# Optimization experiments

Measured on AMD Instinct MI355X. Metric: run time of the kernel, lower is better.

## Reference

```python
import jax, jax.numpy as jnp
import numpy as np
import math

B, L, D = 2, 2048, 512
D_INNER, D_STATE, D_CONV = 2 * D, 16, 4
DT_RANK = math.ceil(D / 16)  # 32


def setup_inputs() -> dict:
    key = jax.random.key(0)
    ks = jax.random.split(key, 9)
    s = 0.02
    x = jax.random.normal(ks[0], (B, L, D), dtype=jnp.float32)
    W_in = jax.random.normal(ks[1], (D, 2 * D_INNER), dtype=jnp.float32) * s
    conv_w = jax.random.normal(ks[2], (D_INNER, D_CONV), dtype=jnp.float32) * s
    conv_b = jnp.zeros((D_INNER,), dtype=jnp.float32)
    W_x = jax.random.normal(ks[3], (D_INNER, DT_RANK + 2 * D_STATE), dtype=jnp.float32) * s
    W_dt = jax.random.normal(ks[4], (DT_RANK, D_INNER), dtype=jnp.float32) * s
    b_dt = jax.random.normal(ks[5], (D_INNER,), dtype=jnp.float32) * s
    # S4D-real init: A = -[1..d_state] per channel
    A_log = jnp.log(jnp.broadcast_to(jnp.arange(1, D_STATE + 1, dtype=jnp.float32), (D_INNER, D_STATE)))
    D_param = jnp.ones((D_INNER,), dtype=jnp.float32)
    W_out = jax.random.normal(ks[6], (D_INNER, D), dtype=jnp.float32) * s
    return {"x": x, "W_in": W_in, "conv_w": conv_w, "conv_b": conv_b,
            "W_x": W_x, "W_dt": W_dt, "b_dt": b_dt, "A_log": A_log,
            "D_param": D_param, "W_out": W_out}


def _mamba(x, W_in, conv_w, conv_b, W_x, W_dt, b_dt, A_log, D_param, W_out):
    # in_proj -> [u, z]
    xz = jnp.einsum('bld,de->ble', x, W_in)
    u, z = jnp.split(xz, 2, axis=-1)  # each (B, L, d_inner)
    # depthwise causal conv1d along L
    u_c = jnp.transpose(u, (0, 2, 1))  # (B, d_inner, L)
    kern = conv_w[:, None, :]          # (d_inner, 1, d_conv)
    u_c = jax.lax.conv_general_dilated(
        u_c, kern, window_strides=(1,), padding=[(D_CONV - 1, 0)],
        feature_group_count=D_INNER,
        dimension_numbers=('NCH', 'OIH', 'NCH')) + conv_b[None, :, None]
    u = jax.nn.silu(jnp.transpose(u_c, (0, 2, 1)))  # (B, L, d_inner)
    # input-dependent dt, B, C
    x_dbl = jnp.einsum('bld,de->ble', u, W_x)
    dt_r = x_dbl[..., :DT_RANK]
    Bm = x_dbl[..., DT_RANK:DT_RANK + D_STATE]          # (B, L, d_state)
    Cm = x_dbl[..., DT_RANK + D_STATE:]                  # (B, L, d_state)
    dt = jax.nn.softplus(jnp.einsum('blr,rd->bld', dt_r, W_dt) + b_dt)  # (B, L, d_inner)
    A = -jnp.exp(A_log)  # (d_inner, d_state)

    def step(h, inp):
        dt_t, B_t, C_t, u_t = inp  # (B,d_inner), (B,d_state), (B,d_state), (B,d_inner)
        dA = jnp.exp(dt_t[:, :, None] * A)                      # (B, d_inner, d_state)
        h = h * dA + (dt_t * u_t)[:, :, None] * B_t[:, None, :]
        y = jnp.einsum('bds,bs->bd', h, C_t)
        return h, y

    h0 = jnp.zeros((B, D_INNER, D_STATE), dtype=x.dtype)
    xs = (jnp.transpose(dt, (1, 0, 2)), jnp.transpose(Bm, (1, 0, 2)),
          jnp.transpose(Cm, (1, 0, 2)), jnp.transpose(u, (1, 0, 2)))
    _, ys = jax.lax.scan(step, h0, xs)
    y = jnp.transpose(ys, (1, 0, 2)) + u * D_param  # (B, L, d_inner)
    y = y * jax.nn.silu(z)
    return jnp.einsum('bld,de->ble', y, W_out)


def reference(x, W_in, conv_w, conv_b, W_x, W_dt, b_dt, A_log, D_param, W_out):
    # MambaLayer.forward (eval): out = x + drop_path(mamba(x)); drop_path == Identity at eval
    return x + _mamba(x, W_in, conv_w, conv_b, W_x, W_dt, b_dt, A_log, D_param, W_out)
```

## Files before the change

### kernel.cpp

```cpp
#include <hip/hip_runtime.h>
#include <math.h>

#define BB 2
#define LL 2048
#define DD 512
#define DIN 1024
#define DXZ 2048
#define DSTATE 16
#define DTRANK 32
#define NDBL 64
#define ML (BB*LL)
#define LC3 32
#define NCH3 64
#define CP3 36
#define PHS 17

typedef __bf16 bf16_t;
typedef bf16_t bf16x8 __attribute__((ext_vector_type(8)));
typedef bf16_t bf16x4 __attribute__((ext_vector_type(4)));
typedef float f32x4 __attribute__((ext_vector_type(4)));

#define GBK 64

typedef const __attribute__((address_space(1))) void* gp1_t;
typedef __attribute__((address_space(3))) void* lp3_t;

__device__ __forceinline__ float fast_silu(float x) {
  return x * __builtin_amdgcn_rcpf(1.f + __builtin_amdgcn_exp2f(-1.44269504f * x));
}

template <int TM, int TN, int MODE, int CT>
__launch_bounds__(256)
__global__ void gemm_mfma(const bf16_t* __restrict__ A,
                          const bf16_t* __restrict__ Bt,
                          float* __restrict__ C, int ldc,
                          int M, int N, int K, int gx,
                          const float* __restrict__ aux) {
  constexpr int ABYTES = 2 * TM * GBK * 2;
  constexpr int BBYTES = 2 * TN * GBK * 2;
  __shared__ __align__(16) char smem[ABYTES + BBYTES];
  bf16_t* As = (bf16_t*)smem;
  bf16_t* Bs = (bf16_t*)(smem + ABYTES);
  const int tid = threadIdx.x;
  const int wid = tid >> 6, lane = tid & 63;
  const int q = lane >> 4, ln = lane & 15;
  constexpr int WM = TM / 2, WN = TN / 2;
  constexpr int FM = WM / 16, FN = WN / 16;
  constexpr int AI = TM * GBK / 2048;
  constexpr int BI = TN * GBK / 2048;
  constexpr int SN = AI + BI;
  const int wm = (wid >> 1) * WM, wn = (wid & 1) * WN;

  const int nwg = gridDim.x;
  const int cpx = nwg >> 3;
  const int o = blockIdx.x;
  const int wg = (o & 7) * cpx + (o >> 3);
  const int bx = wg % gx, by = wg / gx;

  const int mBase = by * TM, nBase = bx * TN;
  const int lr = lane >> 3, lk = (lane & 7) * 8;

  auto stage = [&](int buf, int k0) {
#pragma unroll
    for (int t = 0; t < AI; t++) {
      const int grp = wid * AI + t;
      const bf16_t* g = &A[(size_t)(mBase + grp * 8 + lr) * K + k0 + lk];
      __builtin_amdgcn_global_load_lds((gp1_t)(const void*)g,
                                       (lp3_t)(void*)&As[buf * TM * GBK + grp * 512],
                                       16, 0, 0);
    }
#pragma unroll
    for (int t = 0; t < BI; t++) {
      const int grp = wid * BI + t;
      const bf16_t* g = &Bt[(size_t)(nBase + grp * 8 + lr) * K + k0 + lk];
      __builtin_amdgcn_global_load_lds((gp1_t)(const void*)g,
                                       (lp3_t)(void*)&Bs[buf * TN * GBK + grp * 512],
                                       16, 0, 0);
    }
  };

  f32x4 acc[FM][FN] = {};
  const int NK = K / GBK;
  stage(0, 0);
  stage(1, GBK);
  for (int t = 0; t < NK; t++) {
    const int cur = t & 1;
    if (t < NK - 1) {
      if constexpr (SN == 8)      asm volatile("s_waitcnt vmcnt(8)" ::: "memory");
      else if constexpr (SN == 6) asm volatile("s_waitcnt vmcnt(6)" ::: "memory");
      else if constexpr (SN == 4) asm volatile("s_waitcnt vmcnt(4)" ::: "memory");
      else                        asm volatile("s_waitcnt vmcnt(0)" ::: "memory");
    } else {
      asm volatile("s_waitcnt vmcnt(0)" ::: "memory");
    }
    __builtin_amdgcn_s_barrier();
    __builtin_amdgcn_sched_barrier(0);
    bf16x8 af[FM][2], bfr[FN][2];
#pragma unroll
    for (int i = 0; i < FM; i++)
#pragma unroll
      for (int h = 0; h < 2; h++)
        af[i][h] = *(const bf16x8*)
            &As[cur * TM * GBK + (wm + i * 16 + ln) * GBK + h * 32 + q * 8];
#pragma unroll
    for (int j = 0; j < FN; j++)
#pragma unroll
      for (int h = 0; h < 2; h++)
        bfr[j][h] = *(const bf16x8*)
            &Bs[cur * TN * GBK + (wn + j * 16 + ln) * GBK + h * 32 + q * 8];
#pragma unroll
    for (int i = 0; i < FM; i++)
#pragma unroll
      for (int j = 0; j < FN; j++) {
        acc[i][j] = __builtin_amdgcn_mfma_f32_16x16x32_bf16(
            af[i][0], bfr[j][0], acc[i][j], 0, 0, 0);
        acc[i][j] = __builtin_amdgcn_mfma_f32_16x16x32_bf16(
            af[i][1], bfr[j][1], acc[i][j], 0, 0, 0);
      }
    __builtin_amdgcn_s_barrier();
    __builtin_amdgcn_sched_barrier(0);
    if (t + 2 < NK) stage(cur, (t + 2) * GBK);
  }

  if constexpr (CT == 1) {
    float (*T)[68] = (float(*)[68])smem;
#pragma unroll
    for (int ch = 0; ch < 2; ch++) {
      __syncthreads();
      if ((wid & 1) == ch) {
#pragma unroll
        for (int i = 0; i < FM; i++)
#pragma unroll
          for (int j = 0; j < FN; j++)
            *(f32x4*)&T[j * 16 + ln][wm + i * 16 + q * 4] = acc[i][j];
      }
      __syncthreads();
#pragma unroll
      for (int it = 0; it < 8; it++) {
        const int idx = tid + it * 256;
        const int row = idx >> 5, off = (idx & 31) * 4;
        *(f32x4*)&C[(size_t)(nBase + ch * 64 + row) * ldc + mBase + off] =
            *(const f32x4*)&T[row][off];
      }
    }
  } else {
#pragma unroll
    for (int i = 0; i < FM; i++) {
      const int m0 = mBase + wm + i * 16 + q * 4;
#pragma unroll
      for (int j = 0; j < FN; j++) {
        const int n = nBase + wn + j * 16 + ln;
#pragma unroll
        for (int r = 0; r < 4; r++) {
          float v = acc[i][j][r];
          if (MODE == 2) v += aux[(size_t)(m0 + r) * ldc + n];
          C[(size_t)(m0 + r) * ldc + n] = v;
        }
      }
    }
  }
}

__launch_bounds__(256)
__global__ void prep(const float* __restrict__ x, bf16_t* __restrict__ x_b,
                     const float* __restrict__ W_in, bf16_t* __restrict__ W_inT_b,
                     const float* __restrict__ W_x, bf16_t* __restrict__ W_xT_b,
                     const float* __restrict__ W_out, bf16_t* __restrict__ W_outT_b) {
  __shared__ float T[64][65];
  const int blk = blockIdx.x;
  const int t = threadIdx.x;

  if (blk < 2048) {
    const int i = blk * 256 + t;
    const float4 v = ((const float4*)x)[i];
    bf16x4 o = {(bf16_t)v.x, (bf16_t)v.y, (bf16_t)v.z, (bf16_t)v.w};
    ((bf16x4*)x_b)[i] = o;
    return;
  }
  const float* in;
  bf16_t* out;
  int R, C, bx, by;
  if (blk < 2304) {
    const int k = blk - 2048;
    in = W_in; out = W_inT_b; R = DD; C = DXZ; bx = k & 31; by = k >> 5;
  } else if (blk < 2320) {
    const int k = blk - 2304;
    in = W_x; out = W_xT_b; R = DIN; C = NDBL; bx = 0; by = k;
  } else {
    const int k = blk - 2320;
    in = W_out; out = W_outT_b; R = DIN; C = DD; bx = k & 7; by = k >> 3;
  }
  const int rB = by * 64, cB = bx * 64;
  {
    const int r = t >> 4, c4 = (t & 15) * 4;
#pragma unroll
    for (int i = 0; i < 4; i++) {
      const float4 v = *(const float4*)&in[(size_t)(rB + r + i * 16) * C + cB + c4];
      T[r + i * 16][c4] = v.x;
      T[r + i * 16][c4 + 1] = v.y;
      T[r + i * 16][c4 + 2] = v.z;
      T[r + i * 16][c4 + 3] = v.w;
    }
  }
  __syncthreads();
  {
    const int c = t >> 2;
#pragma unroll
    for (int i = 0; i < 4; i++) {
      const int r0 = (t & 3) * 16 + i * 4;
      bf16x4 o = {(bf16_t)T[r0][c], (bf16_t)T[r0 + 1][c],
                  (bf16_t)T[r0 + 2][c], (bf16_t)T[r0 + 3][c]};
      *(bf16x4*)&out[(size_t)(cB + c) * R + rB + r0] = o;
    }
  }
}

__launch_bounds__(256)
__global__ void transpose_cast(const float* __restrict__ in, bf16_t* __restrict__ out,
                               int R, int C) {
  __shared__ float T[64][65];
  const int t = threadIdx.x;
  const int rB = blockIdx.y * 64, cB = blockIdx.x * 64;
  {
    const int r = t >> 4, c4 = (t & 15) * 4;
#pragma unroll
    for (int i = 0; i < 4; i++) {
      const float4 v = *(const float4*)&in[(size_t)(rB + r + i * 16) * C + cB + c4];
      T[r + i * 16][c4] = v.x;
      T[r + i * 16][c4 + 1] = v.y;
      T[r + i * 16][c4 + 2] = v.z;
      T[r + i * 16][c4 + 3] = v.w;
    }
  }
  __syncthreads();
  {
    const int c = t >> 2;
#pragma unroll
    for (int i = 0; i < 4; i++) {
      const int r0 = (t & 3) * 16 + i * 4;
      bf16x4 o = {(bf16_t)T[r0][c], (bf16_t)T[r0 + 1][c],
                  (bf16_t)T[r0 + 2][c], (bf16_t)T[r0 + 3][c]};
      *(bf16x4*)&out[(size_t)(cB + c) * R + rB + r0] = o;
    }
  }
}

template <int MODE, int AT, int CT>
__launch_bounds__(256)
__global__ void gemm_tiled(const float* __restrict__ A, int lda,
                           const float* __restrict__ B, int ldb,
                           float* __restrict__ C, int ldc,
                           int M, int N, int K,
                           const float* __restrict__ aux) {
  __shared__ float As[16][68];
  __shared__ float Bs[16][68];

  const int tid = threadIdx.x;
  const int tx = tid & 15, ty = tid >> 4;
  const int mBase = blockIdx.y * 64;
  const int nBase = blockIdx.x * 64;

  float acc[4][4] = {};

  for (int k0 = 0; k0 < K; k0 += 16) {
#pragma unroll
    for (int i = 0; i < 4; i++) {
      int idx = tid + i * 256;
      if (AT == 0) {
        int m = idx >> 4, kk = idx & 15;
        As[kk][m] = A[(size_t)(mBase + m) * lda + k0 + kk];
      } else {
        int kk = idx >> 6, m = idx & 63;
        As[kk][m] = A[(size_t)(k0 + kk) * lda + mBase + m];
      }
    }
#pragma unroll
    for (int i = 0; i < 4; i++) {
      int idx = tid + i * 256;
      int kk = idx >> 6, n = idx & 63;
      Bs[kk][n] = B[(size_t)(k0 + kk) * ldb + nBase + n];
    }
    __syncthreads();
#pragma unroll
    for (int kk = 0; kk < 16; kk++) {
      const float4 a4 = *reinterpret_cast<const float4*>(&As[kk][ty * 4]);
      const float4 b4 = *reinterpret_cast<const float4*>(&Bs[kk][tx * 4]);
      const float a[4] = {a4.x, a4.y, a4.z, a4.w};
      const float b[4] = {b4.x, b4.y, b4.z, b4.w};
#pragma unroll
      for (int i = 0; i < 4; i++)
#pragma unroll
        for (int j = 0; j < 4; j++) acc[i][j] = fmaf(a[i], b[j], acc[i][j]);
    }
    __syncthreads();
  }

  if (CT == 0) {
#pragma unroll
    for (int i = 0; i < 4; i++) {
      const int m = mBase + ty * 4 + i;
      const int n0 = nBase + tx * 4;
      float v[4];
#pragma unroll
      for (int j = 0; j < 4; j++) {
        float x = acc[i][j];
        if (MODE == 1) {
          x += aux[n0 + j];
          x = (x > 20.f) ? x
              : 0.69314718f * __builtin_amdgcn_logf(
                    1.f + __builtin_amdgcn_exp2f(x * 1.44269504f));
        }
        v[j] = x;
      }
      *reinterpret_cast<float4*>(&C[(size_t)m * ldc + n0]) =
          make_float4(v[0], v[1], v[2], v[3]);
    }
  } else {
    __shared__ float T3[64][68];
#pragma unroll
    for (int i = 0; i < 4; i++)
#pragma unroll
      for (int j = 0; j < 4; j++) {
        float x = acc[i][j];
        if (MODE == 1) {
          x += aux[nBase + tx * 4 + j];
          x = (x > 20.f) ? x
              : 0.69314718f * __builtin_amdgcn_logf(
                    1.f + __builtin_amdgcn_exp2f(x * 1.44269504f));
        }
        T3[tx * 4 + j][ty * 4 + i] = x;
      }
    __syncthreads();
#pragma unroll
    for (int it = 0; it < 4; it++) {
      const int idx = tid + it * 256;
      const int row = idx >> 4, off = (idx & 15) * 4;
      *(float4*)&C[(size_t)(nBase + row) * ldc + mBase + off] =
          *(const float4*)&T3[row][off];
    }
  }
}

__launch_bounds__(256)
__global__ void conv_silu_T2(const float* __restrict__ xzT,
                             const float* __restrict__ conv_w,
                             const float* __restrict__ conv_b,
                             float* __restrict__ uT,
                             bf16_t* __restrict__ u_b) {
  __shared__ bf16_t T[64][72];
  const int t = threadIdx.x;
  const int d0 = blockIdx.y * 64, ml0 = blockIdx.x * 64;
  const int dd = t >> 2;
  const int m4 = (t & 3) * 16;
  const int d = d0 + dd;
  const float* row = xzT + (size_t)d * ML + ml0 + m4;
  float* orow = uT + (size_t)d * ML + ml0 + m4;
  const float w0 = conv_w[d * 4 + 0], w1 = conv_w[d * 4 + 1];
  const float w2 = conv_w[d * 4 + 2], w3 = conv_w[d * 4 + 3];
  const float bias = conv_b[d];
  const int l0 = (ml0 + m4) & (LL - 1);
  float4 Av = make_float4(0.f, 0.f, 0.f, 0.f);
  if (l0 != 0) Av = *(const float4*)(row - 4);
#pragma unroll
  for (int j = 0; j < 4; j++) {
    const float4 Bv = *(const float4*)(row + j * 4);
    float o0 = bias + w0 * Av.y + w1 * Av.z + w2 * Av.w + w3 * Bv.x;
    float o1 = bias + w0 * Av.z + w1 * Av.w + w2 * Bv.x + w3 * Bv.y;
    float o2 = bias + w0 * Av.w + w1 * Bv.x + w2 * Bv.y + w3 * Bv.z;
    float o3 = bias + w0 * Bv.x + w1 * Bv.y + w2 * Bv.z + w3 * Bv.w;
    o0 = fast_silu(o0); o1 = fast_silu(o1);
    o2 = fast_silu(o2); o3 = fast_silu(o3);
    *(float4*)(orow + j * 4) = make_float4(o0, o1, o2, o3);
    T[m4 + j * 4 + 0][dd] = (bf16_t)o0;
    T[m4 + j * 4 + 1][dd] = (bf16_t)o1;
    T[m4 + j * 4 + 2][dd] = (bf16_t)o2;
    T[m4 + j * 4 + 3][dd] = (bf16_t)o3;
    Av = Bv;
  }
  __syncthreads();
  const int r = t >> 2;
#pragma unroll
  for (int i = 0; i < 2; i++) {
    const int cc = (t & 3) * 16 + i * 8;
    bf16x8 v;
#pragma unroll
    for (int k = 0; k < 8; k++) v[k] = T[r][cc + k];
    *(bf16x8*)&u_b[(size_t)(ml0 + r) * DIN + d0 + cc] = v;
  }
}

__launch_bounds__(256, 4)
__global__ void scan_fused6(const float* __restrict__ dtT,
                            const float* __restrict__ uT,
                            float* __restrict__ xzT,
                            const float* __restrict__ xdbl,
                            const float* __restrict__ A_log,
                            const float* __restrict__ D_param) {
  __shared__ float dt_s[NCH3 * CP3];
  __shared__ float u_s[NCH3 * CP3];
  __shared__ float Pc[NCH3][PHS];
  __shared__ float Hc[NCH3][PHS];

  const int tid = threadIdx.x;
  const int c = blockIdx.x;
  const int b = c >> 10, d = c & (DIN - 1);
  const size_t rowoff = (size_t)d * ML + (size_t)b * LL;
  const float* dtrow = dtT + rowoff;
  const float* urow  = uT + rowoff;
  const float* zrow  = xzT + (size_t)(DIN + d) * ML + (size_t)b * LL;
  float* yrow = xzT + rowoff;

#pragma unroll
  for (int i = 0; i < 2; i++) {
    const int idx = (tid + i * 256) * 4;
    const int la = (idx >> 5) * CP3 + (idx & 31);
    *(float4*)&dt_s[la] = *(const float4*)&dtrow[idx];
    *(float4*)&u_s[la]  = *(const float4*)&urow[idx];
  }

  const int ch = tid >> 2, q = tid & 3;
  const int s0 = q * 4;
  float Al2[4];
#pragma unroll
  for (int k = 0; k < 4; k++)
    Al2[k] = -expf(A_log[d * DSTATE + s0 + k]) * 1.44269504f;
  const float* dp = dt_s + ch * CP3;
  float* up = u_s + ch * CP3;
  const float* BC = xdbl + ((size_t)b * LL + (size_t)ch * LC3) * NDBL + DTRANK + s0;
  __syncthreads();

  {
    float h0 = 0.f, h1 = 0.f, h2 = 0.f, h3 = 0.f, sdt = 0.f;
    float4 Bcur[4];
#pragma unroll
    for (int i = 0; i < 4; i++)
      Bcur[i] = *(const float4*)(BC + (size_t)i * NDBL);
    for (int g = 0; g < 8; g++) {
      float4 Bnxt[4];
#pragma unroll
      for (int i = 0; i < 4; i++)
        Bnxt[i] = *(const float4*)(BC + (size_t)((g + 1) * 4 + i) * NDBL);
#pragma unroll
      for (int i = 0; i < 4; i++) {
        const int l = g * 4 + i;
        const float dtv = dp[l];
        const float dtu = dtv * up[l];
        sdt += dtv;
        const float e0 = __builtin_amdgcn_exp2f(dtv * Al2[0]);
        const float e1 = __builtin_amdgcn_exp2f(dtv * Al2[1]);
        const float e2 = __builtin_amdgcn_exp2f(dtv * Al2[2]);
        const float e3 = __builtin_amdgcn_exp2f(dtv * Al2[3]);
        h0 = fmaf(h0, e0, dtu * Bcur[i].x);
        h1 = fmaf(h1, e1, dtu * Bcur[i].y);
        h2 = fmaf(h2, e2, dtu * Bcur[i].z);
        h3 = fmaf(h3, e3, dtu * Bcur[i].w);
      }
#pragma unroll
      for (int i = 0; i < 4; i++) Bcur[i] = Bnxt[i];
    }
    Pc[ch][s0 + 0] = __builtin_amdgcn_exp2f(Al2[0] * sdt);
    Pc[ch][s0 + 1] = __builtin_amdgcn_exp2f(Al2[1] * sdt);
    Pc[ch][s0 + 2] = __builtin_amdgcn_exp2f(Al2[2] * sdt);
    Pc[ch][s0 + 3] = __builtin_amdgcn_exp2f(Al2[3] * sdt);
    Hc[ch][s0 + 0] = h0;
    Hc[ch][s0 + 1] = h1;
    Hc[ch][s0 + 2] = h2;
    Hc[ch][s0 + 3] = h3;
  }
  __syncthreads();

  if (tid < DSTATE) {
    float h = 0.f;
#pragma unroll
    for (int k = 0; k < NCH3; k++) {
      const float Pv = Pc[k][tid], Hv = Hc[k][tid];
      Pc[k][tid] = h;
      h = fmaf(h, Pv, Hv);
    }
  }
  __syncthreads();

  {
    const float Dp = D_param[d];
    float h0 = Pc[ch][s0], h1 = Pc[ch][s0 + 1];
    float h2 = Pc[ch][s0 + 2], h3 = Pc[ch][s0 + 3];
    float4 Bcur[4], Ccur[4];
#pragma unroll
    for (int i = 0; i < 4; i++) {
      Bcur[i] = *(const float4*)(BC + (size_t)i * NDBL);
      Ccur[i] = *(const float4*)(BC + (size_t)i * NDBL + DSTATE);
    }
    for (int g = 0; g < 8; g++) {
      float4 Bnxt[4], Cnxt[4];
#pragma unroll
      for (int i = 0; i < 4; i++) {
        Bnxt[i] = *(const float4*)(BC + (size_t)((g + 1) * 4 + i) * NDBL);
        Cnxt[i] = *(const float4*)(BC + (size_t)((g + 1) * 4 + i) * NDBL + DSTATE);
      }
#pragma unroll
      for (int i = 0; i < 4; i++) {
        const int l = g * 4 + i;
        const float dtv = dp[l];
        const float uv = up[l];
        const float dtu = dtv * uv;
        const float e0 = __builtin_amdgcn_exp2f(dtv * Al2[0]);
        const float e1 = __builtin_amdgcn_exp2f(dtv * Al2[1]);
        const float e2 = __builtin_amdgcn_exp2f(dtv * Al2[2]);
        const float e3 = __builtin_amdgcn_exp2f(dtv * Al2[3]);
        h0 = fmaf(h0, e0, dtu * Bcur[i].x);
        h1 = fmaf(h1, e1, dtu * Bcur[i].y);
        h2 = fmaf(h2, e2, dtu * Bcur[i].z);
        h3 = fmaf(h3, e3, dtu * Bcur[i].w);
        float p = fmaf(h0, Ccur[i].x,
                  fmaf(h1, Ccur[i].y, fmaf(h2, Ccur[i].z, h3 * Ccur[i].w)));
        p += __int_as_float(__builtin_amdgcn_ds_swizzle(__float_as_int(p), 0x041F));
        p += __int_as_float(__builtin_amdgcn_ds_swizzle(__float_as_int(p), 0x081F));
        if (q == (l & 3)) up[l] = fmaf(uv, Dp, p);
      }
#pragma unroll
      for (int i = 0; i < 4; i++) { Bcur[i] = Bnxt[i]; Ccur[i] = Cnxt[i]; }
    }
  }
  __syncthreads();

#pragma unroll
  for (int i = 0; i < 2; i++) {
    const int idx = (tid + i * 256) * 4;
    const int la = (idx >> 5) * CP3 + (idx & 31);
    const float4 y4 = *(const float4*)&u_s[la];
    const float4 z4 = *(const float4*)&zrow[idx];
    float4 o;
    o.x = y4.x * fast_silu(z4.x);
    o.y = y4.y * fast_silu(z4.y);
    o.z = y4.z * fast_silu(z4.z);
    o.w = y4.w * fast_silu(z4.w);
    *(float4*)&yrow[idx] = o;
  }
}

extern "C" void kernel_launch(void* const* d_in, const int* in_sizes, int n_in,
                              void* d_out, int out_size, void* d_ws, size_t ws_size,
                              hipStream_t stream) {
  const float* x      = (const float*)d_in[0];
  const float* W_in   = (const float*)d_in[1];
  const float* conv_w = (const float*)d_in[2];
  const float* conv_b = (const float*)d_in[3];
  const float* W_x    = (const float*)d_in[4];
  const float* W_dt   = (const float*)d_in[5];
  const float* b_dt   = (const float*)d_in[6];
  const float* A_log  = (const float*)d_in[7];
  const float* D_par  = (const float*)d_in[8];
  const float* W_out  = (const float*)d_in[9];
  float* out = (float*)d_out;

  char* ws = (char*)d_ws;
  float* xzT   = (float*)(ws);
  float* uT    = (float*)(ws + (size_t)ML * DXZ * 4);
  float* x_dbl = (float*)(ws + (size_t)ML * (DXZ + DIN) * 4);
  char* dtT_b  = ws + (size_t)ML * (DXZ + DIN + NDBL) * 4;
  float* dtT   = (float*)dtT_b;
  bf16_t* u_b  = (bf16_t*)dtT_b;
  bf16_t* y_b  = (bf16_t*)(dtT_b + (size_t)ML * DIN * 2);
  char* extra  = ws + (size_t)ML * (DXZ + DIN + NDBL + DIN) * 4;
  bf16_t* x_b      = (bf16_t*)(extra);
  bf16_t* W_inT_b  = (bf16_t*)(extra + (size_t)ML * DD * 2);
  bf16_t* W_outT_b = (bf16_t*)(extra + (size_t)ML * DD * 2 + (size_t)DXZ * DD * 2);
  bf16_t* W_xT_b   = (bf16_t*)(extra + (size_t)ML * DD * 2 + (size_t)DXZ * DD * 2
                               + (size_t)DD * DIN * 2);

  prep<<<2448, 256, 0, stream>>>(x, x_b, W_in, W_inT_b, W_x, W_xT_b,
                                 W_out, W_outT_b);

  gemm_mfma<128, 128, 0, 1><<<512, 256, 0, stream>>>(
      x_b, W_inT_b, xzT, ML, ML, DXZ, DD, 16, nullptr);

  conv_silu_T2<<<dim3(ML / 64, DIN / 64), 256, 0, stream>>>(
      xzT, conv_w, conv_b, uT, u_b);

  gemm_mfma<64, 64, 0, 0><<<64, 256, 0, stream>>>(
      u_b, W_xT_b, x_dbl, NDBL, ML, NDBL, DIN, 1, nullptr);

  gemm_tiled<1, 0, 1><<<dim3(DIN / 64, ML / 64), 256, 0, stream>>>(
      x_dbl, NDBL, W_dt, DIN, dtT, ML, ML, DIN, DTRANK, b_dt);

  scan_fused6<<<BB * DIN, 256, 0, stream>>>(dtT, uT, xzT, x_dbl, A_log, D_par);

  transpose_cast<<<dim3(ML / 64, DIN / 64), 256, 0, stream>>>(xzT, y_b, DIN, ML);

  gemm_mfma<128, 64, 2, 0><<<256, 256, 0, stream>>>(
      y_b, W_outT_b, out, DD, ML, DD, DIN, 8, x);
}
```

Baseline: 192.0 us.

## Fuse dt projection and softplus into the selective scan kernel

Removes the separate tiled GEMM that computed dt and wrote a transposed dt buffer. Each scan block now computes dt for its channel directly from x_dbl rows, W_dt and b_dt, applying softplus before filling shared memory. This eliminates a kernel launch and the global write and read of the dt intermediate. In exchange, every block rereads the dt_rank slice of x_dbl for its batch, which relies on L2 caching, and the per-thread register use for the W_dt column grows.

```diff
diff --git a/kernel.cpp b/kernel.cpp
--- a/kernel.cpp
+++ b/kernel.cpp
@@ -245,102 +245,6 @@
   }
 }
 
-template <int MODE, int AT, int CT>
-__launch_bounds__(256)
-__global__ void gemm_tiled(const float* __restrict__ A, int lda,
-                           const float* __restrict__ B, int ldb,
-                           float* __restrict__ C, int ldc,
-                           int M, int N, int K,
-                           const float* __restrict__ aux) {
-  __shared__ float As[16][68];
-  __shared__ float Bs[16][68];
-
-  const int tid = threadIdx.x;
-  const int tx = tid & 15, ty = tid >> 4;
-  const int mBase = blockIdx.y * 64;
-  const int nBase = blockIdx.x * 64;
-
-  float acc[4][4] = {};
-
-  for (int k0 = 0; k0 < K; k0 += 16) {
-#pragma unroll
-    for (int i = 0; i < 4; i++) {
-      int idx = tid + i * 256;
-      if (AT == 0) {
-        int m = idx >> 4, kk = idx & 15;
-        As[kk][m] = A[(size_t)(mBase + m) * lda + k0 + kk];
-      } else {
-        int kk = idx >> 6, m = idx & 63;
-        As[kk][m] = A[(size_t)(k0 + kk) * lda + mBase + m];
-      }
-    }
-#pragma unroll
-    for (int i = 0; i < 4; i++) {
-      int idx = tid + i * 256;
-      int kk = idx >> 6, n = idx & 63;
-      Bs[kk][n] = B[(size_t)(k0 + kk) * ldb + nBase + n];
-    }
-    __syncthreads();
-#pragma unroll
-    for (int kk = 0; kk < 16; kk++) {
-      const float4 a4 = *reinterpret_cast<const float4*>(&As[kk][ty * 4]);
-      const float4 b4 = *reinterpret_cast<const float4*>(&Bs[kk][tx * 4]);
-      const float a[4] = {a4.x, a4.y, a4.z, a4.w};
-      const float b[4] = {b4.x, b4.y, b4.z, b4.w};
-#pragma unroll
-      for (int i = 0; i < 4; i++)
-#pragma unroll
-        for (int j = 0; j < 4; j++) acc[i][j] = fmaf(a[i], b[j], acc[i][j]);
-    }
-    __syncthreads();
-  }
-
-  if (CT == 0) {
-#pragma unroll
-    for (int i = 0; i < 4; i++) {
-      const int m = mBase + ty * 4 + i;
-      const int n0 = nBase + tx * 4;
-      float v[4];
-#pragma unroll
-      for (int j = 0; j < 4; j++) {
-        float x = acc[i][j];
-        if (MODE == 1) {
-          x += aux[n0 + j];
-          x = (x > 20.f) ? x
-              : 0.69314718f * __builtin_amdgcn_logf(
-                    1.f + __builtin_amdgcn_exp2f(x * 1.44269504f));
-        }
-        v[j] = x;
-      }
-      *reinterpret_cast<float4*>(&C[(size_t)m * ldc + n0]) =
-          make_float4(v[0], v[1], v[2], v[3]);
-    }
-  } else {
-    __shared__ float T3[64][68];
-#pragma unroll
-    for (int i = 0; i < 4; i++)
-#pragma unroll
-      for (int j = 0; j < 4; j++) {
-        float x = acc[i][j];
-        if (MODE == 1) {
-          x += aux[nBase + tx * 4 + j];
-          x = (x > 20.f) ? x
-              : 0.69314718f * __builtin_amdgcn_logf(
-                    1.f + __builtin_amdgcn_exp2f(x * 1.44269504f));
-        }
-        T3[tx * 4 + j][ty * 4 + i] = x;
-      }
-    __syncthreads();
-#pragma unroll
-    for (int it = 0; it < 4; it++) {
-      const int idx = tid + it * 256;
-      const int row = idx >> 4, off = (idx & 15) * 4;
-      *(float4*)&C[(size_t)(nBase + row) * ldc + mBase + off] =
-          *(const float4*)&T3[row][off];
-    }
-  }
-}
-
 __launch_bounds__(256)
 __global__ void conv_silu_T2(const float* __restrict__ xzT,
                              const float* __restrict__ conv_w,
@@ -390,12 +294,13 @@
 }
 
 __launch_bounds__(256, 4)
-__global__ void scan_fused6(const float* __restrict__ dtT,
-                            const float* __restrict__ uT,
-                            float* __restrict__ xzT,
-                            const float* __restrict__ xdbl,
-                            const float* __restrict__ A_log,
-                            const float* __restrict__ D_param) {
+__global__ void scan_fused6b(const float* __restrict__ uT,
+                             float* __restrict__ xzT,
+                             const float* __restrict__ xdbl,
+                             const float* __restrict__ W_dt,
+                             const float* __restrict__ b_dt,
+                             const float* __restrict__ A_log,
+                             const float* __restrict__ D_param) {
   __shared__ float dt_s[NCH3 * CP3];
   __shared__ float u_s[NCH3 * CP3];
   __shared__ float Pc[NCH3][PHS];
@@ -405,7 +310,6 @@
   const int c = blockIdx.x;
   const int b = c >> 10, d = c & (DIN - 1);
   const size_t rowoff = (size_t)d * ML + (size_t)b * LL;
-  const float* dtrow = dtT + rowoff;
   const float* urow  = uT + rowoff;
   const float* zrow  = xzT + (size_t)(DIN + d) * ML + (size_t)b * LL;
   float* yrow = xzT + rowoff;
@@ -414,8 +318,33 @@
   for (int i = 0; i < 2; i++) {
     const int idx = (tid + i * 256) * 4;
     const int la = (idx >> 5) * CP3 + (idx & 31);
-    *(float4*)&dt_s[la] = *(const float4*)&dtrow[idx];
-    *(float4*)&u_s[la]  = *(const float4*)&urow[idx];
+    *(float4*)&u_s[la] = *(const float4*)&urow[idx];
+  }
+
+  {
+    float wdt[DTRANK];
+#pragma unroll
+    for (int r = 0; r < DTRANK; r++) wdt[r] = W_dt[r * DIN + d];
+    const float bdt = b_dt[d];
+    const float* xrow0 = xdbl + (size_t)b * LL * NDBL;
+#pragma unroll
+    for (int j = 0; j < 8; j++) {
+      const int l = tid + j * 256;
+      const float* xr = xrow0 + (size_t)l * NDBL;
+      float a = bdt;
+#pragma unroll
+      for (int r = 0; r < DTRANK; r += 4) {
+        const float4 v = *(const float4*)&xr[r];
+        a = fmaf(v.x, wdt[r], a);
+        a = fmaf(v.y, wdt[r + 1], a);
+        a = fmaf(v.z, wdt[r + 2], a);
+        a = fmaf(v.w, wdt[r + 3], a);
+      }
+      const float dtv = (a > 20.f) ? a
+          : 0.69314718f * __builtin_amdgcn_logf(
+                1.f + __builtin_amdgcn_exp2f(a * 1.44269504f));
+      dt_s[(l >> 5) * CP3 + (l & 31)] = dtv;
+    }
   }
 
   const int ch = tid >> 2, q = tid & 3;
@@ -558,7 +487,6 @@
   float* uT    = (float*)(ws + (size_t)ML * DXZ * 4);
   float* x_dbl = (float*)(ws + (size_t)ML * (DXZ + DIN) * 4);
   char* dtT_b  = ws + (size_t)ML * (DXZ + DIN + NDBL) * 4;
-  float* dtT   = (float*)dtT_b;
   bf16_t* u_b  = (bf16_t*)dtT_b;
   bf16_t* y_b  = (bf16_t*)(dtT_b + (size_t)ML * DIN * 2);
   char* extra  = ws + (size_t)ML * (DXZ + DIN + NDBL + DIN) * 4;
@@ -580,10 +508,8 @@
   gemm_mfma<64, 64, 0, 0><<<64, 256, 0, stream>>>(
       u_b, W_xT_b, x_dbl, NDBL, ML, NDBL, DIN, 1, nullptr);
 
-  gemm_tiled<1, 0, 1><<<dim3(DIN / 64, ML / 64), 256, 0, stream>>>(
-      x_dbl, NDBL, W_dt, DIN, dtT, ML, ML, DIN, DTRANK, b_dt);
-
-  scan_fused6<<<BB * DIN, 256, 0, stream>>>(dtT, uT, xzT, x_dbl, A_log, D_par);
+  scan_fused6b<<<BB * DIN, 256, 0, stream>>>(uT, xzT, x_dbl, W_dt, b_dt,
+                                             A_log, D_par);
 
   transpose_cast<<<dim3(ML / 64, DIN / 64), 256, 0, stream>>>(xzT, y_b, DIN, ML);
 
```

After: 236.1 us. +23.0%, slower.
